# Optimization experiments

Measured on AMD Instinct MI355X. Metric: run time of the kernel, lower is better.

The kernel has to match this reference:

```python
import jax, jax.numpy as jnp
import numpy as np


def setup_inputs() -> dict:
    key = jax.random.key(0)
    ks = jax.random.split(key, 7)
    B, D, H, M, E = 8192, 512, 512, 50, 3
    return {
        "x": jax.random.normal(ks[0], (B, D), dtype=jnp.float32),
        "mem": jax.random.normal(ks[1], (M, D), dtype=jnp.float32),
        "routing_logits": jax.random.normal(ks[2], (E,), dtype=jnp.float32),
        "proj_W": jax.random.normal(ks[3], (H, D), dtype=jnp.float32) * 0.02,
        "proj_b": jax.random.normal(ks[4], (H,), dtype=jnp.float32) * 0.02,
        "ops_W": jax.random.normal(ks[5], (E, H, H), dtype=jnp.float32) * 0.02,
        "ops_b": jax.random.normal(ks[6], (E, H), dtype=jnp.float32) * 0.02,
    }


def reference(x, mem, routing_logits, proj_W, proj_b, ops_W, ops_b):
    # novelty: mean over (batch, memory) of L2 distance between x rows and memory rows
    diff = x[:, None, :] - mem[None, :, :]                 # [B, M, D] -- dominant memory traffic
    novelty = jnp.minimum(1.5, jnp.mean(jnp.linalg.norm(diff, axis=-1)))

    # top-2 routing over softmax of the (per-module, input-independent) logits
    weights = jax.nn.softmax(routing_logits)
    _, top2 = jax.lax.top_k(weights, 2)
    idx_a, idx_b = top2[0], top2[1]

    # operator = ReLU -> Linear(H, H) -> ReLU (torch Linear: y = x @ W.T + b)
    def op(h, W, b):
        return jax.nn.relu(jnp.einsum("bh,oh->bo", jax.nn.relu(h), W) + b)

    x_proj = jnp.einsum("bd,hd->bh", x, proj_W) + proj_b   # [B, H]
    x1 = op(x_proj, ops_W[idx_a], ops_b[idx_a])
    out = op(x1, ops_W[idx_b], ops_b[idx_b])
    return out, novelty
```

## Files before the change

### kernel.cpp

```cpp
#include <hip/hip_runtime.h>

typedef _Float16 f16;
typedef _Float16 f16x8 __attribute__((ext_vector_type(8)));
typedef float f32x4 __attribute__((ext_vector_type(4)));

#define BD 512

__device__ __forceinline__ void llds16(const void* g, void* l) {
  __builtin_amdgcn_global_load_lds(
      (const __attribute__((address_space(1))) unsigned int*)g,
      (__attribute__((address_space(3))) unsigned int*)l,
      16, 0, 0);
}
__device__ __forceinline__ f16x8 cvt8(float4 a, float4 b) {
  f16x8 h;
  h[0]=(f16)a.x; h[1]=(f16)a.y; h[2]=(f16)a.z; h[3]=(f16)a.w;
  h[4]=(f16)b.x; h[5]=(f16)b.y; h[6]=(f16)b.z; h[7]=(f16)b.w;
  return h;
}

__global__ __launch_bounds__(256) void prep_kernel(
    const float* __restrict__ projW, const float* __restrict__ opsW,
    const float* __restrict__ memf, f16* __restrict__ wh,
    f16* __restrict__ memh) {
  const int bid = blockIdx.x, t = threadIdx.x;
  if (bid < 512) {
    const int e = (bid * 256 + t) * 8;
    const float* s = (e < 262144) ? (projW + e) : (opsW + (e - 262144));
    float4 v0 = ((const float4*)s)[0];
    float4 v1 = ((const float4*)s)[1];
    *(f16x8*)&wh[e] = cvt8(v0, v1);
  } else {
    const int e = ((bid - 512) * 256 + t) * 8;
    const int row = e >> 9;
    f16x8 h;
    if (row < 50) {
      float4 v0 = ((const float4*)(memf + e))[0];
      float4 v1 = ((const float4*)(memf + e))[1];
      h = cvt8(v0, v1);
    } else {
      #pragma unroll
      for (int j = 0; j < 8; ++j) h[j] = (f16)0.f;
    }
    *(f16x8*)&memh[e] = h;
  }
}

__global__ __launch_bounds__(256, 2) void gemm1_nov_kernel(
    const float* __restrict__ x, const f16* __restrict__ wh,
    const f16* __restrict__ memh, const float* __restrict__ projB,
    f16* __restrict__ g0, float* __restrict__ novPart) {
  __shared__ __align__(16) char lds[3 * 16384];
  __shared__ float red[4];

  const int t = threadIdx.x, l = t & 63, w = t >> 6;
  const int wr = w >> 1, wc = w & 1;
  const int lr = l & 15, lk = l >> 4;
  const int rowBase = blockIdx.x * 64, colBase = blockIdx.y * 64;
  const bool NOV = (blockIdx.y == 0);

  const int aRow = (t * 16) >> 7;
  const int aCh  = ((t * 16) >> 4) & 7;
  const int bRow = (t * 16) >> 6;
  const int bCh  = ((t * 16) >> 4) & 3;

  auto stage = [&](int buf, int kt) {
    char* base = lds + buf * 16384;
    #pragma unroll
    for (int i = 0; i < 2; ++i) {
      const int row = aRow + i * 32;
      llds16(x + (size_t)(rowBase + row) * BD + kt + ((aCh ^ (row & 7)) * 4),
             base + i * 4096 + w * 1024);
    }
    llds16(wh + (size_t)(colBase + bRow) * BD + kt + ((bCh ^ (bRow & 3)) * 8),
           base + 8192 + w * 1024);
    if (NOV)
      llds16(memh + (size_t)bRow * BD + kt + ((bCh ^ (bRow & 3)) * 8),
             base + 12288 + w * 1024);
  };

  f32x4 acc[2][2], nacc[4];
  #pragma unroll
  for (int m = 0; m < 2; ++m)
    #pragma unroll
    for (int n = 0; n < 2; ++n) acc[m][n] = (f32x4){0.f,0.f,0.f,0.f};
  #pragma unroll
  for (int q = 0; q < 4; ++q) nacc[q] = (f32x4){0.f,0.f,0.f,0.f};
  float xsq[4] = {0.f, 0.f, 0.f, 0.f};
  float msq = 0.f;

  auto readA = [&](const float* Ab, int r) -> f16x8 {
    float4 r0 = *(const float4*)&Ab[r * 32 + (((2 * lk) ^ (r & 7)) << 2)];
    float4 r1 = *(const float4*)&Ab[r * 32 + (((2 * lk + 1) ^ (r & 7)) << 2)];
    return cvt8(r0, r1);
  };

  auto compute = [&](int buf) {
    const float* Ab = (const float*)(lds + buf * 16384);
    const f16* Bb = (const f16*)(lds + buf * 16384 + 8192);
    const f16* Mb = (const f16*)(lds + buf * 16384 + 12288);
    f16x8 af[2], bf[2];
    #pragma unroll
    for (int m = 0; m < 2; ++m) af[m] = readA(Ab, wr * 32 + m * 16 + lr);
    #pragma unroll
    for (int n = 0; n < 2; ++n) {
      const int row = wc * 32 + n * 16 + lr;
      bf[n] = *(const f16x8*)&Bb[row * 32 + ((lk ^ (row & 3)) << 3)];
    }
    __builtin_amdgcn_s_setprio(1);
    #pragma unroll
    for (int m = 0; m < 2; ++m)
      #pragma unroll
      for (int n = 0; n < 2; ++n)
        acc[m][n] = __builtin_amdgcn_mfma_f32_16x16x32_f16(af[m], bf[n], acc[m][n], 0, 0, 0);
    __builtin_amdgcn_s_setprio(0);
    if (NOV) {
      const int mrow = w * 16 + lr;
      f16x8 mf = *(const f16x8*)&Mb[mrow * 32 + ((lk ^ (mrow & 3)) << 3)];
      #pragma unroll
      for (int j = 0; j < 8; ++j) { float f = (float)mf[j]; msq += f * f; }
      f16x8 aq[4];
      if (wr == 0) {
        aq[0] = af[0]; aq[1] = af[1];
        aq[2] = readA(Ab, 32 + lr); aq[3] = readA(Ab, 48 + lr);
      } else {
        aq[0] = readA(Ab, lr); aq[1] = readA(Ab, 16 + lr);
        aq[2] = af[0]; aq[3] = af[1];
      }
      #pragma unroll
      for (int q = 0; q < 4; ++q) {
        #pragma unroll
        for (int j = 0; j < 8; ++j) { float f = (float)aq[q][j]; xsq[q] += f * f; }
        nacc[q] = __builtin_amdgcn_mfma_f32_16x16x32_f16(aq[q], mf, nacc[q], 0, 0, 0);
      }
    }
  };

  stage(0, 0);
  stage(1, 32);
  #pragma unroll
  for (int tt = 0; tt < 16; ++tt) {
    if (NOV) {
      if (tt < 15) asm volatile("s_waitcnt vmcnt(4)" ::: "memory");
      else         asm volatile("s_waitcnt vmcnt(0)" ::: "memory");
    } else {
      if (tt < 15) asm volatile("s_waitcnt vmcnt(3)" ::: "memory");
      else         asm volatile("s_waitcnt vmcnt(0)" ::: "memory");
    }
    __builtin_amdgcn_s_barrier();
    if (tt < 14) stage((tt + 2) % 3, (tt + 2) * 32);
    compute(tt % 3);
    asm volatile("s_waitcnt lgkmcnt(0)" ::: "memory");
  }

  if (NOV) {
    msq += __shfl_xor(msq, 16, 64);
    msq += __shfl_xor(msq, 32, 64);
    #pragma unroll
    for (int q = 0; q < 4; ++q) {
      xsq[q] += __shfl_xor(xsq[q], 16, 64);
      xsq[q] += __shfl_xor(xsq[q], 32, 64);
    }
    const int mm = w * 16 + lr;
    float local = 0.f;
    if (mm < 50) {
      #pragma unroll
      for (int j = 0; j < 4; ++j) {
        const int r16 = lk * 4 + j;
        #pragma unroll
        for (int q = 0; q < 4; ++q) {
          const float xs = __shfl(xsq[q], r16, 64);
          float d = xs - 2.f * nacc[q][j] + msq;
          local += sqrtf(fmaxf(d, 0.f));
        }
      }
    }
    #pragma unroll
    for (int off = 32; off; off >>= 1) local += __shfl_down(local, off, 64);
    if (l == 0) red[w] = local;
    __syncthreads();
    if (t == 0) novPart[blockIdx.x] = red[0] + red[1] + red[2] + red[3];
  }

  #pragma unroll
  for (int n = 0; n < 2; ++n) {
    const int col = colBase + wc * 32 + n * 16 + lr;
    const float bbv = projB[col];
    #pragma unroll
    for (int m = 0; m < 2; ++m) {
      #pragma unroll
      for (int j = 0; j < 4; ++j) {
        const int rowg = rowBase + wr * 32 + m * 16 + lk * 4 + j;
        g0[(size_t)rowg * BD + col] = (f16)fmaxf(acc[m][n][j] + bbv, 0.f);
      }
    }
  }
}

template <int PICK, int OUTF16>
__global__ __launch_bounds__(256, 2) void gemm_relu_kernel(
    const f16* __restrict__ A, const f16* __restrict__ Wall,
    const float* __restrict__ ball, const float* __restrict__ logits,
    void* __restrict__ Out, const float* __restrict__ novPart,
    float* __restrict__ novOut) {
  __shared__ __align__(16) char lds[4 * 16384];

  const int t = threadIdx.x;
  const int l = t & 63;
  const int w = t >> 6;
  const int wr = w >> 1, wc = w & 1;
  const int lr = l & 15, lk = l >> 4;

  if (PICK == 2 && blockIdx.x == 0 && blockIdx.y == 0 && w == 0) {
    float s = novPart[l] + novPart[l + 64];
    #pragma unroll
    for (int off = 32; off; off >>= 1) s += __shfl_down(s, off, 64);
    if (l == 0) novOut[0] = fminf(1.5f, s * (1.0f / (8192.0f * 50.0f)));
  }

  float l0 = logits[0], l1 = logits[1], l2 = logits[2];
  int ia = 0; float ba = l0;
  if (l1 > ba) { ba = l1; ia = 1; }
  if (l2 > ba) { ba = l2; ia = 2; }
  int widx;
  if (PICK == 1) {
    widx = ia;
  } else {
    int ib = 0; float bb2 = -3.4e38f;
    if (ia != 0)             { bb2 = l0; ib = 0; }
    if (ia != 1 && l1 > bb2) { bb2 = l1; ib = 1; }
    if (ia != 2 && l2 > bb2) { bb2 = l2; ib = 2; }
    widx = ib;
  }
  const f16* W = Wall + (size_t)widx * BD * BD;
  const float* bias = ball + widx * BD;

  const int rowBase = blockIdx.x * 64;
  const int colBase = blockIdx.y * 64;

  f32x4 acc[2][2];
  #pragma unroll
  for (int m = 0; m < 2; ++m)
    #pragma unroll
    for (int n = 0; n < 2; ++n) acc[m][n] = (f32x4){0.f, 0.f, 0.f, 0.f};

  auto stage = [&](int buf, int kt) {
    f16* Ab = (f16*)(lds + buf * 16384);
    f16* Bb = (f16*)(lds + buf * 16384 + 8192);
    #pragma unroll
    for (int i = 0; i < 2; ++i) {
      const int o = i * 4096 + t * 16;
      const int row = o >> 7;
      const int sch = ((o >> 4) & 7) ^ (row & 7);
      llds16(A + (size_t)(rowBase + row) * BD + kt + sch * 8,
             (char*)Ab + i * 4096 + w * 1024);
      llds16(W + (size_t)(colBase + row) * BD + kt + sch * 8,
             (char*)Bb + i * 4096 + w * 1024);
    }
  };

  auto compute = [&](int buf) {
    const f16* Ab = (const f16*)(lds + buf * 16384);
    const f16* Bb = (const f16*)(lds + buf * 16384 + 8192);
    #pragma unroll
    for (int kk = 0; kk < 64; kk += 32) {
      const int ch = (kk >> 3) + lk;
      f16x8 af[2], bf[2];
      #pragma unroll
      for (int m = 0; m < 2; ++m) {
        const int row = wr * 32 + m * 16 + lr;
        af[m] = *(const f16x8*)&Ab[row * 64 + ((ch ^ (row & 7)) << 3)];
      }
      #pragma unroll
      for (int n = 0; n < 2; ++n) {
        const int row = wc * 32 + n * 16 + lr;
        bf[n] = *(const f16x8*)&Bb[row * 64 + ((ch ^ (row & 7)) << 3)];
      }
      __builtin_amdgcn_s_setprio(1);
      #pragma unroll
      for (int m = 0; m < 2; ++m)
        #pragma unroll
        for (int n = 0; n < 2; ++n)
          acc[m][n] = __builtin_amdgcn_mfma_f32_16x16x32_f16(af[m], bf[n], acc[m][n], 0, 0, 0);
      __builtin_amdgcn_s_setprio(0);
    }
  };

  stage(0, 0);
  stage(1, 64);
  stage(2, 128);
  #pragma unroll
  for (int t8 = 0; t8 < 8; ++t8) {
    if (t8 < 6)       asm volatile("s_waitcnt vmcnt(8)" ::: "memory");
    else if (t8 == 6) asm volatile("s_waitcnt vmcnt(4)" ::: "memory");
    else              asm volatile("s_waitcnt vmcnt(0)" ::: "memory");
    __builtin_amdgcn_s_barrier();
    if (t8 < 5) stage((t8 + 3) & 3, (t8 + 3) * 64);
    compute(t8 & 3);
    asm volatile("s_waitcnt lgkmcnt(0)" ::: "memory");
  }

  #pragma unroll
  for (int n = 0; n < 2; ++n) {
    const int col = colBase + wc * 32 + n * 16 + lr;
    const float bbv = bias[col];
    #pragma unroll
    for (int m = 0; m < 2; ++m) {
      #pragma unroll
      for (int j = 0; j < 4; ++j) {
        const int rowg = rowBase + wr * 32 + m * 16 + lk * 4 + j;
        float v = fmaxf(acc[m][n][j] + bbv, 0.f);
        if (OUTF16) ((f16*)Out)[(size_t)rowg * BD + col] = (f16)v;
        else        ((float*)Out)[(size_t)rowg * BD + col] = v;
      }
    }
  }
}

extern "C" void kernel_launch(void* const* d_in, const int* in_sizes, int n_in,
                              void* d_out, int out_size, void* d_ws, size_t ws_size,
                              hipStream_t stream) {
  const float* x      = (const float*)d_in[0];
  const float* memf   = (const float*)d_in[1];
  const float* logits = (const float*)d_in[2];
  const float* projW  = (const float*)d_in[3];
  const float* projB  = (const float*)d_in[4];
  const float* opsW   = (const float*)d_in[5];
  const float* opsB   = (const float*)d_in[6];
  float* out = (float*)d_out;

  char* ws = (char*)d_ws;
  f16*   g0      = (f16*)(ws);
  f16*   h1      = (f16*)(ws + 8388608);
  f16*   wh      = (f16*)(ws + 16777216);
  f16*   memh    = (f16*)(ws + 18874368);
  float* novPart = (float*)(ws + 18939904);

  prep_kernel<<<528, 256, 0, stream>>>(projW, opsW, memf, wh, memh);

  gemm1_nov_kernel<<<dim3(128, 8), 256, 0, stream>>>(x, wh, memh, projB, g0, novPart);
  gemm_relu_kernel<1, 1><<<dim3(128, 8), 256, 0, stream>>>(
      g0, wh + 262144, opsB, logits, (void*)h1, novPart, out + 4194304);
  gemm_relu_kernel<2, 0><<<dim3(128, 8), 256, 0, stream>>>(
      h1, wh + 262144, opsB, logits, (void*)out, novPart, out + 4194304);
}
```

Before: 48.38 us.

## Pre-convert x to fp16, widen K tile to 64, remap blocks across XCDs

The prep kernel now also converts x to fp16, so the first GEMM streams half-width A data and no longer converts in the inner loop. The first GEMM's K step grows from 32 to 64 with three larger LDS buffers and eight iterations instead of sixteen. All GEMMs remap block IDs so consecutive row panels land on the same XCD for better L2 reuse. The trade-off is an extra full pass over x (read fp32, write fp16) in a separate kernel, plus a larger LDS footprint that may lower occupancy.

```diff
diff --git a/kernel.cpp b/kernel.cpp
--- a/kernel.cpp
+++ b/kernel.cpp
@@ -19,19 +19,31 @@
   return h;
 }
 
+__device__ __forceinline__ void remap_xcd(int lid, int& rowPanel, int& colPanel) {
+  const int xcd = lid & 7;
+  const int j = lid >> 3;
+  rowPanel = (j & 15) * 8 + xcd;
+  colPanel = j >> 4;
+}
+
 __global__ __launch_bounds__(256) void prep_kernel(
-    const float* __restrict__ projW, const float* __restrict__ opsW,
-    const float* __restrict__ memf, f16* __restrict__ wh,
-    f16* __restrict__ memh) {
+    const float* __restrict__ x, const float* __restrict__ projW,
+    const float* __restrict__ opsW, const float* __restrict__ memf,
+    f16* __restrict__ xh, f16* __restrict__ wh, f16* __restrict__ memh) {
   const int bid = blockIdx.x, t = threadIdx.x;
-  if (bid < 512) {
+  if (bid < 2048) {
     const int e = (bid * 256 + t) * 8;
+    float4 v0 = ((const float4*)(x + e))[0];
+    float4 v1 = ((const float4*)(x + e))[1];
+    *(f16x8*)&xh[e] = cvt8(v0, v1);
+  } else if (bid < 2560) {
+    const int e = ((bid - 2048) * 256 + t) * 8;
     const float* s = (e < 262144) ? (projW + e) : (opsW + (e - 262144));
     float4 v0 = ((const float4*)s)[0];
     float4 v1 = ((const float4*)s)[1];
     *(f16x8*)&wh[e] = cvt8(v0, v1);
   } else {
-    const int e = ((bid - 512) * 256 + t) * 8;
+    const int e = ((bid - 2560) * 256 + t) * 8;
     const int row = e >> 9;
     f16x8 h;
     if (row < 50) {
@@ -47,36 +59,42 @@
 }
 
 __global__ __launch_bounds__(256, 2) void gemm1_nov_kernel(
-    const float* __restrict__ x, const f16* __restrict__ wh,
+    const f16* __restrict__ A, const f16* __restrict__ wh,
     const f16* __restrict__ memh, const float* __restrict__ projB,
     f16* __restrict__ g0, float* __restrict__ novPart) {
-  __shared__ __align__(16) char lds[3 * 16384];
+  __shared__ __align__(16) char lds[3 * 24576];
   __shared__ float red[4];
 
   const int t = threadIdx.x, l = t & 63, w = t >> 6;
   const int wr = w >> 1, wc = w & 1;
   const int lr = l & 15, lk = l >> 4;
-  const int rowBase = blockIdx.x * 64, colBase = blockIdx.y * 64;
-  const bool NOV = (blockIdx.y == 0);
-
-  const int aRow = (t * 16) >> 7;
-  const int aCh  = ((t * 16) >> 4) & 7;
-  const int bRow = (t * 16) >> 6;
-  const int bCh  = ((t * 16) >> 4) & 3;
+  int rowPanel, colPanel;
+  remap_xcd(blockIdx.y * 128 + blockIdx.x, rowPanel, colPanel);
+  const int rowBase = rowPanel * 64, colBase = colPanel * 64;
+  const bool NOV = (colPanel == 0);
 
   auto stage = [&](int buf, int kt) {
-    char* base = lds + buf * 16384;
+    char* base = lds + buf * 24576;
     #pragma unroll
     for (int i = 0; i < 2; ++i) {
-      const int row = aRow + i * 32;
-      llds16(x + (size_t)(rowBase + row) * BD + kt + ((aCh ^ (row & 7)) * 4),
+      const int o = i * 4096 + t * 16;
+      const int row = o >> 7;
+      const int sch = ((o >> 4) & 7) ^ (row & 7);
+      llds16(A + (size_t)(rowBase + row) * BD + kt + sch * 8,
              base + i * 4096 + w * 1024);
-    }
-    llds16(wh + (size_t)(colBase + bRow) * BD + kt + ((bCh ^ (bRow & 3)) * 8),
-           base + 8192 + w * 1024);
-    if (NOV)
-      llds16(memh + (size_t)bRow * BD + kt + ((bCh ^ (bRow & 3)) * 8),
-             base + 12288 + w * 1024);
+      llds16(wh + (size_t)(colBase + row) * BD + kt + sch * 8,
+             base + 8192 + i * 4096 + w * 1024);
+    }
+    if (NOV) {
+      #pragma unroll
+      for (int i = 0; i < 2; ++i) {
+        const int o = i * 4096 + t * 16;
+        const int row = o >> 7;
+        const int sch = ((o >> 4) & 7) ^ (row & 7);
+        llds16(memh + (size_t)row * BD + kt + sch * 8,
+               base + 16384 + i * 4096 + w * 1024);
+      }
+    }
   };
 
   f32x4 acc[2][2], nacc[4];
@@ -89,67 +107,67 @@
   float xsq[4] = {0.f, 0.f, 0.f, 0.f};
   float msq = 0.f;
 
-  auto readA = [&](const float* Ab, int r) -> f16x8 {
-    float4 r0 = *(const float4*)&Ab[r * 32 + (((2 * lk) ^ (r & 7)) << 2)];
-    float4 r1 = *(const float4*)&Ab[r * 32 + (((2 * lk + 1) ^ (r & 7)) << 2)];
-    return cvt8(r0, r1);
+  auto compute = [&](int buf) {
+    const f16* Ab = (const f16*)(lds + buf * 24576);
+    const f16* Bb = (const f16*)(lds + buf * 24576 + 8192);
+    const f16* Mb = (const f16*)(lds + buf * 24576 + 16384);
+    #pragma unroll
+    for (int kk = 0; kk < 64; kk += 32) {
+      const int ch = (kk >> 3) + lk;
+      auto readA = [&](int r) -> f16x8 {
+        return *(const f16x8*)&Ab[r * 64 + ((ch ^ (r & 7)) << 3)];
+      };
+      f16x8 af[2], bf[2];
+      #pragma unroll
+      for (int m = 0; m < 2; ++m) af[m] = readA(wr * 32 + m * 16 + lr);
+      #pragma unroll
+      for (int n = 0; n < 2; ++n) {
+        const int row = wc * 32 + n * 16 + lr;
+        bf[n] = *(const f16x8*)&Bb[row * 64 + ((ch ^ (row & 7)) << 3)];
+      }
+      __builtin_amdgcn_s_setprio(1);
+      #pragma unroll
+      for (int m = 0; m < 2; ++m)
+        #pragma unroll
+        for (int n = 0; n < 2; ++n)
+          acc[m][n] = __builtin_amdgcn_mfma_f32_16x16x32_f16(af[m], bf[n], acc[m][n], 0, 0, 0);
+      __builtin_amdgcn_s_setprio(0);
+      if (NOV) {
+        const int mrow = w * 16 + lr;
+        f16x8 mf = *(const f16x8*)&Mb[mrow * 64 + ((ch ^ (mrow & 7)) << 3)];
+        #pragma unroll
+        for (int j = 0; j < 8; ++j) { float f = (float)mf[j]; msq += f * f; }
+        f16x8 aq[4];
+        if (wr == 0) {
+          aq[0] = af[0]; aq[1] = af[1];
+          aq[2] = readA(32 + lr); aq[3] = readA(48 + lr);
+        } else {
+          aq[0] = readA(lr); aq[1] = readA(16 + lr);
+          aq[2] = af[0]; aq[3] = af[1];
+        }
+        #pragma unroll
+        for (int q = 0; q < 4; ++q) {
+          #pragma unroll
+          for (int j = 0; j < 8; ++j) { float f = (float)aq[q][j]; xsq[q] += f * f; }
+          nacc[q] = __builtin_amdgcn_mfma_f32_16x16x32_f16(aq[q], mf, nacc[q], 0, 0, 0);
+        }
+      }
+    }
   };
 
-  auto compute = [&](int buf) {
-    const float* Ab = (const float*)(lds + buf * 16384);
-    const f16* Bb = (const f16*)(lds + buf * 16384 + 8192);
-    const f16* Mb = (const f16*)(lds + buf * 16384 + 12288);
-    f16x8 af[2], bf[2];
-    #pragma unroll
-    for (int m = 0; m < 2; ++m) af[m] = readA(Ab, wr * 32 + m * 16 + lr);
-    #pragma unroll
-    for (int n = 0; n < 2; ++n) {
-      const int row = wc * 32 + n * 16 + lr;
-      bf[n] = *(const f16x8*)&Bb[row * 32 + ((lk ^ (row & 3)) << 3)];
-    }
-    __builtin_amdgcn_s_setprio(1);
-    #pragma unroll
-    for (int m = 0; m < 2; ++m)
-      #pragma unroll
-      for (int n = 0; n < 2; ++n)
-        acc[m][n] = __builtin_amdgcn_mfma_f32_16x16x32_f16(af[m], bf[n], acc[m][n], 0, 0, 0);
-    __builtin_amdgcn_s_setprio(0);
-    if (NOV) {
-      const int mrow = w * 16 + lr;
-      f16x8 mf = *(const f16x8*)&Mb[mrow * 32 + ((lk ^ (mrow & 3)) << 3)];
-      #pragma unroll
-      for (int j = 0; j < 8; ++j) { float f = (float)mf[j]; msq += f * f; }
-      f16x8 aq[4];
-      if (wr == 0) {
-        aq[0] = af[0]; aq[1] = af[1];
-        aq[2] = readA(Ab, 32 + lr); aq[3] = readA(Ab, 48 + lr);
-      } else {
-        aq[0] = readA(Ab, lr); aq[1] = readA(Ab, 16 + lr);
-        aq[2] = af[0]; aq[3] = af[1];
-      }
-      #pragma unroll
-      for (int q = 0; q < 4; ++q) {
-        #pragma unroll
-        for (int j = 0; j < 8; ++j) { float f = (float)aq[q][j]; xsq[q] += f * f; }
-        nacc[q] = __builtin_amdgcn_mfma_f32_16x16x32_f16(aq[q], mf, nacc[q], 0, 0, 0);
-      }
-    }
-  };
-
   stage(0, 0);
-  stage(1, 32);
-  #pragma unroll
-  for (int tt = 0; tt < 16; ++tt) {
-    if (NOV) {
-      if (tt < 15) asm volatile("s_waitcnt vmcnt(4)" ::: "memory");
-      else         asm volatile("s_waitcnt vmcnt(0)" ::: "memory");
+  stage(1, 64);
+  #pragma unroll
+  for (int t8 = 0; t8 < 8; ++t8) {
+    if (t8 < 7) {
+      if (NOV) asm volatile("s_waitcnt vmcnt(6)" ::: "memory");
+      else     asm volatile("s_waitcnt vmcnt(4)" ::: "memory");
     } else {
-      if (tt < 15) asm volatile("s_waitcnt vmcnt(3)" ::: "memory");
-      else         asm volatile("s_waitcnt vmcnt(0)" ::: "memory");
+      asm volatile("s_waitcnt vmcnt(0)" ::: "memory");
     }
     __builtin_amdgcn_s_barrier();
-    if (tt < 14) stage((tt + 2) % 3, (tt + 2) * 32);
-    compute(tt % 3);
+    if (t8 < 6) stage((t8 + 2) % 3, (t8 + 2) * 64);
+    compute(t8 % 3);
     asm volatile("s_waitcnt lgkmcnt(0)" ::: "memory");
   }
 
@@ -179,7 +197,7 @@
     for (int off = 32; off; off >>= 1) local += __shfl_down(local, off, 64);
     if (l == 0) red[w] = local;
     __syncthreads();
-    if (t == 0) novPart[blockIdx.x] = red[0] + red[1] + red[2] + red[3];
+    if (t == 0) novPart[rowPanel] = red[0] + red[1] + red[2] + red[3];
   }
 
   #pragma unroll
@@ -235,8 +253,10 @@
   const f16* W = Wall + (size_t)widx * BD * BD;
   const float* bias = ball + widx * BD;
 
-  const int rowBase = blockIdx.x * 64;
-  const int colBase = blockIdx.y * 64;
+  int rowPanel, colPanel;
+  remap_xcd(blockIdx.y * 128 + blockIdx.x, rowPanel, colPanel);
+  const int rowBase = rowPanel * 64;
+  const int colBase = colPanel * 64;
 
   f32x4 acc[2][2];
   #pragma unroll
@@ -330,17 +350,17 @@
   float* out = (float*)d_out;
 
   char* ws = (char*)d_ws;
-  f16*   g0      = (f16*)(ws);
-  f16*   h1      = (f16*)(ws + 8388608);
+  f16*   xh      = (f16*)(ws);
+  f16*   g0      = (f16*)(ws + 8388608);
   f16*   wh      = (f16*)(ws + 16777216);
   f16*   memh    = (f16*)(ws + 18874368);
   float* novPart = (float*)(ws + 18939904);
 
-  prep_kernel<<<528, 256, 0, stream>>>(projW, opsW, memf, wh, memh);
-
-  gemm1_nov_kernel<<<dim3(128, 8), 256, 0, stream>>>(x, wh, memh, projB, g0, novPart);
+  prep_kernel<<<2576, 256, 0, stream>>>(x, projW, opsW, memf, xh, wh, memh);
+
+  gemm1_nov_kernel<<<dim3(128, 8), 256, 0, stream>>>(xh, wh, memh, projB, g0, novPart);
   gemm_relu_kernel<1, 1><<<dim3(128, 8), 256, 0, stream>>>(
-      g0, wh + 262144, opsB, logits, (void*)h1, novPart, out + 4194304);
+      g0, wh + 262144, opsB, logits, (void*)xh, novPart, out + 4194304);
   gemm_relu_kernel<2, 0><<<dim3(128, 8), 256, 0, stream>>>(
-      h1, wh + 262144, opsB, logits, (void*)out, novPart, out + 4194304);
-}
+      xh, wh + 262144, opsB, logits, (void*)out, novPart, out + 4194304);
+}
```

Measured after the change: 45.91 us. 1.05x faster.

## Switch GEMM1 pipeline to double-buffered BK=64 tiles with wider swizzle

Applied to the files above, without the earlier changes.

The gemm1+novelty kernel goes from a triple-buffered K=32 pipeline to a double-buffered K=64 pipeline, with two MFMA sub-steps per stage and a 16-way or 8-way XOR swizzle on the wider LDS rows. This halves the number of barrier iterations and issues larger loads per stage. In exchange it waits for all loads to finish (vmcnt(0)) each iteration, so there is less prefetch depth. LDS use also grows from 48KB to 64KB per block, which may affect the two-blocks-per-CU target.

```diff
diff --git a/kernel.cpp b/kernel.cpp
--- a/kernel.cpp
+++ b/kernel.cpp
@@ -50,7 +50,7 @@
     const float* __restrict__ x, const f16* __restrict__ wh,
     const f16* __restrict__ memh, const float* __restrict__ projB,
     f16* __restrict__ g0, float* __restrict__ novPart) {
-  __shared__ __align__(16) char lds[3 * 16384];
+  __shared__ __align__(16) char lds[2 * 32768];
   __shared__ float red[4];
 
   const int t = threadIdx.x, l = t & 63, w = t >> 6;
@@ -59,24 +59,34 @@
   const int rowBase = blockIdx.x * 64, colBase = blockIdx.y * 64;
   const bool NOV = (blockIdx.y == 0);
 
-  const int aRow = (t * 16) >> 7;
-  const int aCh  = ((t * 16) >> 4) & 7;
-  const int bRow = (t * 16) >> 6;
-  const int bCh  = ((t * 16) >> 4) & 3;
-
   auto stage = [&](int buf, int kt) {
-    char* base = lds + buf * 16384;
+    char* base = lds + buf * 32768;
+    #pragma unroll
+    for (int i = 0; i < 4; ++i) {
+      const int o = i * 4096 + t * 16;
+      const int row = o >> 8;
+      const int sch = ((o >> 4) & 15) ^ (row & 15);
+      llds16(x + (size_t)(rowBase + row) * BD + kt + sch * 4,
+             base + i * 4096 + w * 1024);
+    }
     #pragma unroll
     for (int i = 0; i < 2; ++i) {
-      const int row = aRow + i * 32;
-      llds16(x + (size_t)(rowBase + row) * BD + kt + ((aCh ^ (row & 7)) * 4),
-             base + i * 4096 + w * 1024);
-    }
-    llds16(wh + (size_t)(colBase + bRow) * BD + kt + ((bCh ^ (bRow & 3)) * 8),
-           base + 8192 + w * 1024);
-    if (NOV)
-      llds16(memh + (size_t)bRow * BD + kt + ((bCh ^ (bRow & 3)) * 8),
-             base + 12288 + w * 1024);
+      const int o = i * 4096 + t * 16;
+      const int row = o >> 7;
+      const int sch = ((o >> 4) & 7) ^ (row & 7);
+      llds16(wh + (size_t)(colBase + row) * BD + kt + sch * 8,
+             base + 16384 + i * 4096 + w * 1024);
+    }
+    if (NOV) {
+      #pragma unroll
+      for (int i = 0; i < 2; ++i) {
+        const int o = i * 4096 + t * 16;
+        const int row = o >> 7;
+        const int sch = ((o >> 4) & 7) ^ (row & 7);
+        llds16(memh + (size_t)row * BD + kt + sch * 8,
+               base + 24576 + i * 4096 + w * 1024);
+      }
+    }
   };
 
   f32x4 acc[2][2], nacc[4];
@@ -89,67 +99,65 @@
   float xsq[4] = {0.f, 0.f, 0.f, 0.f};
   float msq = 0.f;
 
-  auto readA = [&](const float* Ab, int r) -> f16x8 {
-    float4 r0 = *(const float4*)&Ab[r * 32 + (((2 * lk) ^ (r & 7)) << 2)];
-    float4 r1 = *(const float4*)&Ab[r * 32 + (((2 * lk + 1) ^ (r & 7)) << 2)];
-    return cvt8(r0, r1);
+  auto compute = [&](int buf) {
+    const float* Ab = (const float*)(lds + buf * 32768);
+    const f16* Bb = (const f16*)(lds + buf * 32768 + 16384);
+    const f16* Mb = (const f16*)(lds + buf * 32768 + 24576);
+    #pragma unroll
+    for (int kk = 0; kk < 64; kk += 32) {
+      auto readA = [&](int r) -> f16x8 {
+        const int c0 = ((kk >> 2) + 2 * lk) ^ (r & 15);
+        const int c1 = ((kk >> 2) + 2 * lk + 1) ^ (r & 15);
+        float4 r0 = *(const float4*)&Ab[r * 64 + c0 * 4];
+        float4 r1 = *(const float4*)&Ab[r * 64 + c1 * 4];
+        return cvt8(r0, r1);
+      };
+      const int ch = (kk >> 3) + lk;
+      f16x8 af[2], bf[2];
+      #pragma unroll
+      for (int m = 0; m < 2; ++m) af[m] = readA(wr * 32 + m * 16 + lr);
+      #pragma unroll
+      for (int n = 0; n < 2; ++n) {
+        const int row = wc * 32 + n * 16 + lr;
+        bf[n] = *(const f16x8*)&Bb[row * 64 + ((ch ^ (row & 7)) << 3)];
+      }
+      __builtin_amdgcn_s_setprio(1);
+      #pragma unroll
+      for (int m = 0; m < 2; ++m)
+        #pragma unroll
+        for (int n = 0; n < 2; ++n)
+          acc[m][n] = __builtin_amdgcn_mfma_f32_16x16x32_f16(af[m], bf[n], acc[m][n], 0, 0, 0);
+      __builtin_amdgcn_s_setprio(0);
+      if (NOV) {
+        const int mrow = w * 16 + lr;
+        f16x8 mf = *(const f16x8*)&Mb[mrow * 64 + ((ch ^ (mrow & 7)) << 3)];
+        #pragma unroll
+        for (int j = 0; j < 8; ++j) { float f = (float)mf[j]; msq += f * f; }
+        f16x8 aq[4];
+        if (wr == 0) {
+          aq[0] = af[0]; aq[1] = af[1];
+          aq[2] = readA(32 + lr); aq[3] = readA(48 + lr);
+        } else {
+          aq[0] = readA(lr); aq[1] = readA(16 + lr);
+          aq[2] = af[0]; aq[3] = af[1];
+        }
+        #pragma unroll
+        for (int q = 0; q < 4; ++q) {
+          #pragma unroll
+          for (int j = 0; j < 8; ++j) { float f = (float)aq[q][j]; xsq[q] += f * f; }
+          nacc[q] = __builtin_amdgcn_mfma_f32_16x16x32_f16(aq[q], mf, nacc[q], 0, 0, 0);
+        }
+      }
+    }
   };
 
-  auto compute = [&](int buf) {
-    const float* Ab = (const float*)(lds + buf * 16384);
-    const f16* Bb = (const f16*)(lds + buf * 16384 + 8192);
-    const f16* Mb = (const f16*)(lds + buf * 16384 + 12288);
-    f16x8 af[2], bf[2];
-    #pragma unroll
-    for (int m = 0; m < 2; ++m) af[m] = readA(Ab, wr * 32 + m * 16 + lr);
-    #pragma unroll
-    for (int n = 0; n < 2; ++n) {
-      const int row = wc * 32 + n * 16 + lr;
-      bf[n] = *(const f16x8*)&Bb[row * 32 + ((lk ^ (row & 3)) << 3)];
-    }
-    __builtin_amdgcn_s_setprio(1);
-    #pragma unroll
-    for (int m = 0; m < 2; ++m)
-      #pragma unroll
-      for (int n = 0; n < 2; ++n)
-        acc[m][n] = __builtin_amdgcn_mfma_f32_16x16x32_f16(af[m], bf[n], acc[m][n], 0, 0, 0);
-    __builtin_amdgcn_s_setprio(0);
-    if (NOV) {
-      const int mrow = w * 16 + lr;
-      f16x8 mf = *(const f16x8*)&Mb[mrow * 32 + ((lk ^ (mrow & 3)) << 3)];
-      #pragma unroll
-      for (int j = 0; j < 8; ++j) { float f = (float)mf[j]; msq += f * f; }
-      f16x8 aq[4];
-      if (wr == 0) {
-        aq[0] = af[0]; aq[1] = af[1];
-        aq[2] = readA(Ab, 32 + lr); aq[3] = readA(Ab, 48 + lr);
-      } else {
-        aq[0] = readA(Ab, lr); aq[1] = readA(Ab, 16 + lr);
-        aq[2] = af[0]; aq[3] = af[1];
-      }
-      #pragma unroll
-      for (int q = 0; q < 4; ++q) {
-        #pragma unroll
-        for (int j = 0; j < 8; ++j) { float f = (float)aq[q][j]; xsq[q] += f * f; }
-        nacc[q] = __builtin_amdgcn_mfma_f32_16x16x32_f16(aq[q], mf, nacc[q], 0, 0, 0);
-      }
-    }
-  };
-
   stage(0, 0);
-  stage(1, 32);
-  #pragma unroll
-  for (int tt = 0; tt < 16; ++tt) {
-    if (NOV) {
-      if (tt < 15) asm volatile("s_waitcnt vmcnt(4)" ::: "memory");
-      else         asm volatile("s_waitcnt vmcnt(0)" ::: "memory");
-    } else {
-      if (tt < 15) asm volatile("s_waitcnt vmcnt(3)" ::: "memory");
-      else         asm volatile("s_waitcnt vmcnt(0)" ::: "memory");
-    }
+  #pragma unroll
+  for (int t8 = 0; t8 < 8; ++t8) {
+    asm volatile("s_waitcnt vmcnt(0)" ::: "memory");
     __builtin_amdgcn_s_barrier();
-    if (tt < 14) stage((tt + 2) % 3, (tt + 2) * 32);
-    compute(tt % 3);
+    if (t8 < 7) stage((t8 + 1) & 1, (t8 + 1) * 64);
+    compute(t8 & 1);
     asm volatile("s_waitcnt lgkmcnt(0)" ::: "memory");
   }
 
```

After: 50.82 us. 5.0% more time.
